# Kernel tuning notes

Hardware: AMD Instinct MI355X
Metric: run time of the kernel (lower is better)

Reference implementation:

```python
import jax, jax.numpy as jnp
import numpy as np

EMB_DIM = 768
NUM_HEADS = 12
OUT_DIM = 768


def setup_inputs() -> dict:
    key = jax.random.key(0)
    k_x, k_q, k_k, k_v, k_o = jax.random.split(key, 5)
    B, N, D = 8, 1024, EMB_DIM
    s = 1.0 / np.sqrt(D)
    return {
        "x": jax.random.normal(k_x, (B, N, D), dtype=jnp.float32),
        # torch nn.Linear weights are stored [out_features, in_features]
        "Wq": jax.random.normal(k_q, (D, D), dtype=jnp.float32) * s,
        "Wk": jax.random.normal(k_k, (D, D), dtype=jnp.float32) * s,
        "Wv": jax.random.normal(k_v, (D, D), dtype=jnp.float32) * s,
        "Wo": jax.random.normal(k_o, (OUT_DIM, D), dtype=jnp.float32) * s,
    }


def _split_heads(t, H):
    # [B, N, D] -> [B*H, N, D//H]  (heads folded into batch, per einsum 'b i d')
    B, N, D = t.shape
    return t.reshape(B, N, H, D // H).transpose(0, 2, 1, 3).reshape(B * H, N, D // H)


def _merge_heads(t, B, H):
    BH, N, dh = t.shape
    return t.reshape(B, H, N, dh).transpose(0, 2, 1, 3).reshape(B, N, H * dh)


def reference(x, Wq, Wk, Wv, Wo):
    B, N, D = x.shape
    H = NUM_HEADS
    dh = D // H
    # q/k/v projections (torch Linear: y = x @ W.T, no bias)
    q = _split_heads(x @ Wq.T, H)
    k = _split_heads(x @ Wk.T, H)
    v = _split_heads(x @ Wv.T, H)
    scale = dh ** (-0.5)
    # dots: 'b i d , b j d -> b i j' -> full [B*H, N, N] score matrix
    dots = jnp.einsum('bid,bjd->bij', q, k) * scale
    attn = jax.nn.softmax(dots, axis=-1)
    # dropout p=0.0 -> identity
    # vect: 'b i d , b d j -> b i j' == attn @ v
    vect = jnp.einsum('bij,bjd->bid', attn, v)
    out = _merge_heads(vect, B, H) @ Wo.T
    return out
```

## Files before the change

### kernel.cpp

```cpp
#include <hip/hip_runtime.h>
#include <hip/hip_bf16.h>
#include <stdint.h>


typedef __bf16 bf16x8 __attribute__((ext_vector_type(8)));
typedef __bf16 bf16x4 __attribute__((ext_vector_type(4)));
typedef float f32x4 __attribute__((ext_vector_type(4)));

#define GAS __attribute__((address_space(1)))
#define LAS __attribute__((address_space(3)))

__device__ __forceinline__ void glds16(const short* gp, short* lp) {
  __builtin_amdgcn_global_load_lds((const GAS void*)gp, (LAS void*)lp, 16, 0, 0);
}

__device__ __forceinline__ float fast_exp2(float x) {
#if __has_builtin(__builtin_amdgcn_exp2f)
  return __builtin_amdgcn_exp2f(x);
#else
  return __expf(x * 0.6931471805599453f);
#endif
}

__device__ __forceinline__ short bfbits(float f) {
  __bf16 b = (__bf16)f;
  union { __bf16 b; short s; } cv; cv.b = b;
  return cv.s;
}

__device__ __forceinline__ void stage8_f32(const float* __restrict__ src, short* dst) {
  float4 f0 = ((const float4*)src)[0];
  float4 f1 = ((const float4*)src)[1];
  bf16x8 t;
  t[0] = (__bf16)f0.x; t[1] = (__bf16)f0.y; t[2] = (__bf16)f0.z; t[3] = (__bf16)f0.w;
  t[4] = (__bf16)f1.x; t[5] = (__bf16)f1.y; t[6] = (__bf16)f1.z; t[7] = (__bf16)f1.w;
  *(bf16x8*)dst = t;
}

__global__ __launch_bounds__(256) void convert_kernel(
    const float* __restrict__ x, const float* __restrict__ Wq,
    const float* __restrict__ Wk, const float* __restrict__ Wv,
    const float* __restrict__ Wo,
    short* __restrict__ xb, short* __restrict__ wqkv, short* __restrict__ wob) {
  int u0 = blockIdx.x * 1024 + threadIdx.x;
#pragma unroll
  for (int i = 0; i < 4; ++i) {
    int u = u0 + i * 256;
    const float* src; short* dst;
    if (u < 786432) { src = x + (size_t)u * 8; dst = xb + (size_t)u * 8; }
    else if (u < 1007616) {
      int r = u - 786432;
      int wsel = r / 73728, off = r % 73728;
      const float* W = (wsel == 0) ? Wq : (wsel == 1) ? Wk : Wv;
      src = W + (size_t)off * 8;
      dst = wqkv + (size_t)r * 8;
    } else {
      int r = u - 1007616;
      src = Wo + (size_t)r * 8; dst = wob + (size_t)r * 8;
    }
    stage8_f32(src, dst);
  }
}

__device__ __forceinline__ void stage_half(const short* __restrict__ g, short* l,
                                           int w, int lane) {
#pragma unroll
  for (int p = 0; p < 2; ++p) {
    int c = (w * 2 + p) * 64 + lane;
    int row = c >> 3;
    int cs = ((c & 7) ^ (row & 7)) * 8;
    glds16(g + (size_t)row * 768 + cs, l + c * 8);
  }
}

__device__ __forceinline__ void stage_b192(const short* __restrict__ g, short* l,
                                           int w, int lane) {
#pragma unroll
  for (int p = 0; p < 3; ++p) {
    int c = (w * 3 + p) * 64 + lane;
    int row = c >> 3;
    int cs = ((c & 7) ^ (row & 7)) * 8;
    glds16(g + (size_t)row * 768 + cs, l + c * 8);
  }
}

__device__ __forceinline__ void bar_fence() {
  asm volatile("" ::: "memory");
  __builtin_amdgcn_s_barrier();
  asm volatile("" ::: "memory");
}

__device__ __forceinline__ void load_a8(const short* base, int wr, int l16, int quad,
                                        bf16x8 (&fa)[4][2]) {
#pragma unroll
  for (int mf = 0; mf < 4; ++mf)
#pragma unroll
    for (int kk = 0; kk < 2; ++kk) {
      int row = wr * 64 + mf * 16 + l16;
      fa[mf][kk] = *(const bf16x8*)&base[row * 64 + ((((kk << 2) + quad) ^ (row & 7)) << 3)];
    }
}

__device__ __forceinline__ void load_b4(const short* base, int rbase, int l16, int quad,
                                        bf16x8 (&fb)[2][2]) {
#pragma unroll
  for (int nf = 0; nf < 2; ++nf)
#pragma unroll
    for (int kk = 0; kk < 2; ++kk) {
      int row = rbase + nf * 16 + l16;
      fb[nf][kk] = *(const bf16x8*)&base[row * 64 + ((((kk << 2) + quad) ^ (row & 7)) << 3)];
    }
}

__device__ __forceinline__ void load_b2(const short* base, int rbase, int l16, int quad,
                                        bf16x8 (&fb)[2]) {
#pragma unroll
  for (int kk = 0; kk < 2; ++kk) {
    int row = rbase + l16;
    fb[kk] = *(const bf16x8*)&base[row * 64 + ((((kk << 2) + quad) ^ (row & 7)) << 3)];
  }
}

__device__ __forceinline__ void mma16(const bf16x8 (&fa)[4][2], const bf16x8 (&fb)[2][2],
                                      f32x4 (&acc)[4][4], int nf0) {
  __builtin_amdgcn_s_setprio(1);
#pragma unroll
  for (int kk = 0; kk < 2; ++kk)
#pragma unroll
    for (int mf = 0; mf < 4; ++mf)
#pragma unroll
      for (int nf = 0; nf < 2; ++nf)
        acc[mf][nf0 + nf] = __builtin_amdgcn_mfma_f32_16x16x32_bf16(
            fa[mf][kk], fb[nf][kk], acc[mf][nf0 + nf], 0, 0, 0);
  __builtin_amdgcn_s_setprio(0);
}

__device__ __forceinline__ void mma16o(const bf16x8 (&fa)[4][2], const bf16x8 (&fb)[2][2],
                                       f32x4 (&acc)[4][3]) {
  __builtin_amdgcn_s_setprio(1);
#pragma unroll
  for (int kk = 0; kk < 2; ++kk)
#pragma unroll
    for (int mf = 0; mf < 4; ++mf)
#pragma unroll
      for (int nf = 0; nf < 2; ++nf)
        acc[mf][nf] = __builtin_amdgcn_mfma_f32_16x16x32_bf16(
            fa[mf][kk], fb[nf][kk], acc[mf][nf], 0, 0, 0);
  __builtin_amdgcn_s_setprio(0);
}

__device__ __forceinline__ void mma8o(const bf16x8 (&fa)[4][2], const bf16x8 (&fb)[2],
                                      f32x4 (&acc)[4][3]) {
  __builtin_amdgcn_s_setprio(1);
#pragma unroll
  for (int kk = 0; kk < 2; ++kk)
#pragma unroll
    for (int mf = 0; mf < 4; ++mf)
      acc[mf][2] = __builtin_amdgcn_mfma_f32_16x16x32_bf16(
          fa[mf][kk], fb[kk], acc[mf][2], 0, 0, 0);
  __builtin_amdgcn_s_setprio(0);
}

__global__ __launch_bounds__(512, 4) void gemm_qkv(
    const short* __restrict__ xb, const short* __restrict__ wqkv,
    short* __restrict__ q, short* __restrict__ k, short* __restrict__ vt) {
  const int lin = blockIdx.x;
  const int xcd = lin & 7, grp = lin >> 3;
  const int by = grp >> 3;
  const int bx = xcd * 8 + (grp & 7);
  const int m0 = bx * 128;
  const int n0g = by * 256;
  const int tid = threadIdx.x;
  const int w = tid >> 6, lane = tid & 63, l16 = lane & 15, quad = lane >> 4;
  const int wr = w >> 2, wc = w & 3;

  __shared__ short sA[8192];
  __shared__ short sB[16384];

  const short* Asrc = xb + (size_t)m0 * 768;
  const short* Bsrc = wqkv + (size_t)n0g * 768;

  f32x4 acc[4][4];
#pragma unroll
  for (int i = 0; i < 4; ++i)
#pragma unroll
    for (int j = 0; j < 4; ++j) acc[i][j] = (f32x4){0.f, 0.f, 0.f, 0.f};

  const int bh = wc >> 1;
  const int rb0 = (wc & 1) * 64;

  for (int t = 0; t < 12; ++t) {
    __syncthreads();
    stage_half(Asrc + (size_t)t * 64, sA, w, lane);
    stage_half(Bsrc + (size_t)t * 64, sB, w, lane);
    stage_half(Bsrc + 98304 + (size_t)t * 64, &sB[8192], w, lane);
    __syncthreads();
    bf16x8 fa[4][2], fb0[2][2], fb1[2][2];
    load_a8(sA, wr, l16, quad, fa);
    load_b4(&sB[bh * 8192], rb0, l16, quad, fb0);
    mma16(fa, fb0, acc, 0);
    load_b4(&sB[bh * 8192], rb0 + 32, l16, quad, fb1);
    mma16(fa, fb1, acc, 2);
  }

  const int wsel = by / 3;
  const int nl0 = (by % 3) * 256 + wc * 64;
  if (wsel == 2) {
#pragma unroll
    for (int mf = 0; mf < 4; ++mf)
#pragma unroll
      for (int nf = 0; nf < 4; ++nf) {
        int token = m0 + wr * 64 + mf * 16 + quad * 4;
        int nl = nl0 + nf * 16 + l16;
        int bhh = (token >> 10) * 12 + (nl >> 6);
        int jt = (token >> 7) & 7;
        int fb = (wr * 2 + (mf >> 1)) * 4 + nf;
        short tmp[4];
#pragma unroll
        for (int r = 0; r < 4; ++r) tmp[r] = bfbits(acc[mf][nf][r]);
        *(uint2*)(vt + (size_t)bhh * 65536 + jt * 8192 + fb * 512 +
                  (l16 + 16 * quad) * 8 + (mf & 1) * 4) = *(const uint2*)tmp;
      }
  } else {
    short* C = wsel ? k : q;
    const float sc = wsel ? 1.0f : 0.1803368801111244f;
#pragma unroll
    for (int mf = 0; mf < 4; ++mf)
#pragma unroll
      for (int nf = 0; nf < 4; ++nf)
#pragma unroll
        for (int r = 0; r < 4; ++r) {
          int row = m0 + wr * 64 + mf * 16 + quad * 4 + r;
          int nl = nl0 + nf * 16 + l16;
          C[(size_t)row * 768 + nl] = bfbits(acc[mf][nf][r] * sc);
        }
  }
}

__device__ __forceinline__ void attn_stage_k(const short* __restrict__ kb, int j0,
                                             short* sK, int w, int lane) {
#pragma unroll
  for (int p = 0; p < 4; ++p) {
    int lin = (w * 4 + p) * 64 + lane;
    int row = lin >> 3;
    int cs = ((lin & 7) ^ (row & 7)) * 8;
    glds16(kb + (size_t)(j0 + row) * 768 + cs, &sK[lin * 8]);
  }
}

__device__ __forceinline__ void attn_stage_v(const short* __restrict__ vb, int jt,
                                             short* sVt, int w, int lane) {
#pragma unroll
  for (int p = 0; p < 4; ++p) {
    int c = (w * 4 + p) * 64 + lane;
    glds16(vb + (size_t)jt * 8192 + (size_t)c * 8, &sVt[c * 8]);
  }
}

__global__ __launch_bounds__(256, 3) void attn_kernel(
    const short* __restrict__ q, const short* __restrict__ k,
    const short* __restrict__ vt, short* __restrict__ vect) {
  const int bh = blockIdx.x % 96;
  const int qt = blockIdx.x / 96;
  const int b = bh / 12, h = bh % 12;
  const int m0 = qt * 128;
  const int tid = threadIdx.x;
  const int w = tid >> 6, lane = tid & 63, l16 = lane & 15, quad = lane >> 4;

  __shared__ short sK[128 * 64];
  __shared__ short sVt[64 * 128];

  const size_t base = (size_t)b * 786432 + (size_t)h * 64;
  const short* kb = k + base;
  const short* vb = vt + (size_t)bh * 65536;

#pragma unroll
  for (int p = 0; p < 4; ++p) {
    int lin = (w * 4 + p) * 64 + lane;
    int row = lin >> 3;
    int cs = ((lin & 7) ^ (row & 7)) * 8;
    glds16(q + base + (size_t)(m0 + row) * 768 + cs, &sK[lin * 8]);
  }
  asm volatile("s_waitcnt vmcnt(0)" ::: "memory");
  bar_fence();
  bf16x8 bq[2][2];
#pragma unroll
  for (int g = 0; g < 2; ++g)
#pragma unroll
    for (int kk = 0; kk < 2; ++kk) {
      int row = g * 64 + w * 16 + l16;
      bq[g][kk] = *(const bf16x8*)&sK[row * 64 + (((kk * 4 + quad) ^ (row & 7)) << 3)];
    }
  asm volatile("s_waitcnt lgkmcnt(0)" ::: "memory");
  __builtin_amdgcn_sched_barrier(0);
  bar_fence();

  attn_stage_k(kb, 0, sK, w, lane);
  attn_stage_v(vb, 0, sVt, w, lane);

  f32x4 l4[2];
  l4[0] = (f32x4){0.f, 0.f, 0.f, 0.f};
  l4[1] = (f32x4){0.f, 0.f, 0.f, 0.f};
  f32x4 oacc[2][4];
#pragma unroll
  for (int g = 0; g < 2; ++g)
#pragma unroll
    for (int td = 0; td < 4; ++td) oacc[g][td] = (f32x4){0.f, 0.f, 0.f, 0.f};

  for (int jt = 0; jt < 8; ++jt) {
    asm volatile("s_waitcnt vmcnt(4)" ::: "memory");
    bar_fence();

    bf16x4 pb[2][2][4];
#pragma unroll
    for (int jh = 0; jh < 2; ++jh) {
      f32x4 s[2][4];
#pragma unroll
      for (int g = 0; g < 2; ++g)
#pragma unroll
        for (int ti = 0; ti < 4; ++ti) s[g][ti] = (f32x4){0.f, 0.f, 0.f, 0.f};
      __builtin_amdgcn_s_setprio(1);
#pragma unroll
      for (int kk = 0; kk < 2; ++kk)
#pragma unroll
        for (int ti = 0; ti < 4; ++ti) {
          int row = jh * 64 + ti * 16 + l16;
          bf16x8 a = *(const bf16x8*)&sK[row * 64 + (((kk * 4 + quad) ^ (row & 7)) << 3)];
          s[0][ti] = __builtin_amdgcn_mfma_f32_16x16x32_bf16(a, bq[0][kk], s[0][ti], 0, 0, 0);
          s[1][ti] = __builtin_amdgcn_mfma_f32_16x16x32_bf16(a, bq[1][kk], s[1][ti], 0, 0, 0);
        }
      __builtin_amdgcn_s_setprio(0);
#pragma unroll
      for (int g = 0; g < 2; ++g)
#pragma unroll
        for (int ti = 0; ti < 4; ++ti) {
          f32x4 e;
          e[0] = fast_exp2(s[g][ti][0]);
          e[1] = fast_exp2(s[g][ti][1]);
          e[2] = fast_exp2(s[g][ti][2]);
          e[3] = fast_exp2(s[g][ti][3]);
          l4[g] += e;
          bf16x4 tb;
          tb[0] = (__bf16)e[0]; tb[1] = (__bf16)e[1];
          tb[2] = (__bf16)e[2]; tb[3] = (__bf16)e[3];
          pb[jh][g][ti] = tb;
        }
    }
    asm volatile("s_waitcnt lgkmcnt(0)" ::: "memory");
    __builtin_amdgcn_sched_barrier(0);
    bar_fence();
    if (jt < 7) attn_stage_k(kb, (jt + 1) * 128, sK, w, lane);

    if (jt < 7) { asm volatile("s_waitcnt vmcnt(4)" ::: "memory"); }
    else        { asm volatile("s_waitcnt vmcnt(0)" ::: "memory"); }
    bar_fence();

    __builtin_amdgcn_s_setprio(1);
#pragma unroll
    for (int jh = 0; jh < 2; ++jh)
#pragma unroll
      for (int t2 = 0; t2 < 2; ++t2) {
        union { bf16x4 hh[2]; bf16x8 v; } bp0, bp1;
        bp0.hh[0] = pb[jh][0][2 * t2];
        bp0.hh[1] = pb[jh][0][2 * t2 + 1];
        bp1.hh[0] = pb[jh][1][2 * t2];
        bp1.hh[1] = pb[jh][1][2 * t2 + 1];
        const int fb = (jh * 2 + t2) * 4;
#pragma unroll
        for (int td = 0; td < 4; ++td) {
          bf16x8 av = *(const bf16x8*)&sVt[(fb + td) * 512 + lane * 8];
          oacc[0][td] = __builtin_amdgcn_mfma_f32_16x16x32_bf16(av, bp0.v, oacc[0][td], 0, 0, 0);
          oacc[1][td] = __builtin_amdgcn_mfma_f32_16x16x32_bf16(av, bp1.v, oacc[1][td], 0, 0, 0);
        }
      }
    __builtin_amdgcn_s_setprio(0);
    asm volatile("s_waitcnt lgkmcnt(0)" ::: "memory");
    __builtin_amdgcn_sched_barrier(0);
    bar_fence();
    if (jt < 7) attn_stage_v(vb, jt + 1, sVt, w, lane);
  }

#pragma unroll
  for (int g = 0; g < 2; ++g) {
    float l = (l4[g][0] + l4[g][1]) + (l4[g][2] + l4[g][3]);
    l += __shfl_xor(l, 16);
    l += __shfl_xor(l, 32);
    float inv = 1.0f / l;
    int i_tok = m0 + g * 64 + w * 16 + l16;
#pragma unroll
    for (int td = 0; td < 4; ++td) {
      short tmp[4];
#pragma unroll
      for (int r = 0; r < 4; ++r) tmp[r] = bfbits(oacc[g][td][r] * inv);
      *(uint2*)(vect + base + (size_t)i_tok * 768 + td * 16 + quad * 4) = *(const uint2*)tmp;
    }
  }
}

__global__ __launch_bounds__(512, 2) void gemm_out(
    const short* __restrict__ vect, const short* __restrict__ wob,
    float* __restrict__ out) {
  const int lin = blockIdx.x;
  const int xcd = lin & 7, grp = lin >> 3;
  const int by = grp >> 3;
  const int bx = xcd * 8 + (grp & 7);
  const int m0 = bx * 128;
  const int n0g = by * 192;
  const int tid = threadIdx.x;
  const int w = tid >> 6, lane = tid & 63, l16 = lane & 15, quad = lane >> 4;
  const int wr = w >> 2, wc = w & 3;

  __shared__ short lds[3][20480];

  const short* Asrc = vect + (size_t)m0 * 768;
  const short* Bsrc = wob + (size_t)n0g * 768;

  f32x4 acc[4][3];
#pragma unroll
  for (int i = 0; i < 4; ++i)
#pragma unroll
    for (int j = 0; j < 3; ++j) acc[i][j] = (f32x4){0.f, 0.f, 0.f, 0.f};

  stage_half(Asrc, &lds[0][0], w, lane);
  stage_b192(Bsrc, &lds[0][8192], w, lane);
  stage_half(Asrc + 64, &lds[1][0], w, lane);
  stage_b192(Bsrc + 64, &lds[1][8192], w, lane);
  asm volatile("s_waitcnt vmcnt(5)" ::: "memory");
  bar_fence();

  const int rb0 = wc * 48;
  bf16x8 fa[4][2], fb01[2][2], fb2[2];

#pragma unroll
  for (int t = 0; t < 12; ++t) {
    const int buf = t % 3, nb = (t + 2) % 3;
    const bool pf = (t < 10);
    const short* A = &lds[buf][0];
    const short* Bb = &lds[buf][8192];

    load_a8(A, wr, l16, quad, fa);
    load_b4(Bb, rb0, l16, quad, fb01);
    if (pf) stage_half(Asrc + (size_t)(t + 2) * 64, &lds[nb][0], w, lane);
    bar_fence();
    __builtin_amdgcn_sched_barrier(0);
    mma16o(fa, fb01, acc);
    __builtin_amdgcn_sched_barrier(0);
    bar_fence();

    load_b2(Bb, rb0 + 32, l16, quad, fb2);
    if (pf) {
      stage_b192(Bsrc + (size_t)(t + 2) * 64, &lds[nb][8192], w, lane);
      asm volatile("s_waitcnt vmcnt(5)" ::: "memory");
    } else if (t == 10) {
      asm volatile("s_waitcnt vmcnt(0)" ::: "memory");
    }
    bar_fence();
    __builtin_amdgcn_sched_barrier(0);
    mma8o(fa, fb2, acc);
    __builtin_amdgcn_sched_barrier(0);
    bar_fence();
  }

#pragma unroll
  for (int mf = 0; mf < 4; ++mf)
#pragma unroll
    for (int nf = 0; nf < 3; ++nf)
#pragma unroll
      for (int r = 0; r < 4; ++r) {
        int row = m0 + wr * 64 + mf * 16 + quad * 4 + r;
        int col = n0g + wc * 48 + nf * 16 + l16;
        out[(size_t)row * 768 + col] = acc[mf][nf][r];
      }
}

extern "C" void kernel_launch(void* const* d_in, const int* in_sizes, int n_in,
                              void* d_out, int out_size, void* d_ws, size_t ws_size,
                              hipStream_t stream) {
  const float* x  = (const float*)d_in[0];
  const float* Wq = (const float*)d_in[1];
  const float* Wk = (const float*)d_in[2];
  const float* Wv = (const float*)d_in[3];
  const float* Wo = (const float*)d_in[4];
  float* out = (float*)d_out;

  const size_t MN = (size_t)8192 * 768;
  short* q    = (short*)d_ws;
  short* k    = q + MN;
  short* vt   = k + MN;
  short* vect = q;
  short* wob  = vt + MN;

  short* xb   = (short*)d_out;
  short* wqkv = xb + MN;

  convert_kernel<<<1056, 256, 0, stream>>>(x, Wq, Wk, Wv, Wo, xb, wqkv, wob);
  gemm_qkv<<<576, 512, 0, stream>>>(xb, wqkv, q, k, vt);
  attn_kernel<<<768, 256, 0, stream>>>(q, k, vt, vect);
  gemm_out<<<256, 512, 0, stream>>>(vect, wob, out);
}
```

Baseline: 170.5 us.

## Load V fragments directly from global into registers, dropping V LDS staging

The V tile is no longer staged through shared memory. Each wave now reads its pre-swizzled V fragments straight from global memory into registers before the PV MFMAs. This halves LDS use, which allows higher occupancy, and removes two barriers per iteration. In exchange, V global loads are no longer prefetched a tile ahead, so their latency is exposed, and every wave re-reads the same V data through cache.

```diff
diff --git a/kernel.cpp b/kernel.cpp
--- a/kernel.cpp
+++ b/kernel.cpp
@@ -248,15 +248,6 @@
   }
 }
 
-__device__ __forceinline__ void attn_stage_v(const short* __restrict__ vb, int jt,
-                                             short* sVt, int w, int lane) {
-#pragma unroll
-  for (int p = 0; p < 4; ++p) {
-    int c = (w * 4 + p) * 64 + lane;
-    glds16(vb + (size_t)jt * 8192 + (size_t)c * 8, &sVt[c * 8]);
-  }
-}
-
 __global__ __launch_bounds__(256, 3) void attn_kernel(
     const short* __restrict__ q, const short* __restrict__ k,
     const short* __restrict__ vt, short* __restrict__ vect) {
@@ -268,7 +259,6 @@
   const int w = tid >> 6, lane = tid & 63, l16 = lane & 15, quad = lane >> 4;
 
   __shared__ short sK[128 * 64];
-  __shared__ short sVt[64 * 128];
 
   const size_t base = (size_t)b * 786432 + (size_t)h * 64;
   const short* kb = k + base;
@@ -296,7 +286,6 @@
   bar_fence();
 
   attn_stage_k(kb, 0, sK, w, lane);
-  attn_stage_v(vb, 0, sVt, w, lane);
 
   f32x4 l4[2];
   l4[0] = (f32x4){0.f, 0.f, 0.f, 0.f};
@@ -308,7 +297,7 @@
     for (int td = 0; td < 4; ++td) oacc[g][td] = (f32x4){0.f, 0.f, 0.f, 0.f};
 
   for (int jt = 0; jt < 8; ++jt) {
-    asm volatile("s_waitcnt vmcnt(4)" ::: "memory");
+    asm volatile("s_waitcnt vmcnt(0)" ::: "memory");
     bar_fence();
 
     bf16x4 pb[2][2][4];
@@ -349,15 +338,18 @@
     asm volatile("s_waitcnt lgkmcnt(0)" ::: "memory");
     __builtin_amdgcn_sched_barrier(0);
     bar_fence();
-    if (jt < 7) attn_stage_k(kb, (jt + 1) * 128, sK, w, lane);
-
-    if (jt < 7) { asm volatile("s_waitcnt vmcnt(4)" ::: "memory"); }
-    else        { asm volatile("s_waitcnt vmcnt(0)" ::: "memory"); }
-    bar_fence();
-
-    __builtin_amdgcn_s_setprio(1);
-#pragma unroll
-    for (int jh = 0; jh < 2; ++jh)
+
+    const short* vj = vb + (size_t)jt * 8192;
+#pragma unroll
+    for (int jh = 0; jh < 2; ++jh) {
+      bf16x8 av[2][4];
+#pragma unroll
+      for (int t2 = 0; t2 < 2; ++t2)
+#pragma unroll
+        for (int td = 0; td < 4; ++td)
+          av[t2][td] = *(const bf16x8*)(vj + ((jh * 2 + t2) * 4 + td) * 512 + lane * 8);
+      if (jh == 0 && jt < 7) attn_stage_k(kb, (jt + 1) * 128, sK, w, lane);
+      __builtin_amdgcn_s_setprio(1);
 #pragma unroll
       for (int t2 = 0; t2 < 2; ++t2) {
         union { bf16x4 hh[2]; bf16x8 v; } bp0, bp1;
@@ -365,19 +357,14 @@
         bp0.hh[1] = pb[jh][0][2 * t2 + 1];
         bp1.hh[0] = pb[jh][1][2 * t2];
         bp1.hh[1] = pb[jh][1][2 * t2 + 1];
-        const int fb = (jh * 2 + t2) * 4;
 #pragma unroll
         for (int td = 0; td < 4; ++td) {
-          bf16x8 av = *(const bf16x8*)&sVt[(fb + td) * 512 + lane * 8];
-          oacc[0][td] = __builtin_amdgcn_mfma_f32_16x16x32_bf16(av, bp0.v, oacc[0][td], 0, 0, 0);
-          oacc[1][td] = __builtin_amdgcn_mfma_f32_16x16x32_bf16(av, bp1.v, oacc[1][td], 0, 0, 0);
+          oacc[0][td] = __builtin_amdgcn_mfma_f32_16x16x32_bf16(av[t2][td], bp0.v, oacc[0][td], 0, 0, 0);
+          oacc[1][td] = __builtin_amdgcn_mfma_f32_16x16x32_bf16(av[t2][td], bp1.v, oacc[1][td], 0, 0, 0);
         }
       }
-    __builtin_amdgcn_s_setprio(0);
-    asm volatile("s_waitcnt lgkmcnt(0)" ::: "memory");
-    __builtin_amdgcn_sched_barrier(0);
-    bar_fence();
-    if (jt < 7) attn_stage_v(vb, jt + 1, sVt, w, lane);
+      __builtin_amdgcn_s_setprio(0);
+    }
   }
 
 #pragma unroll
```

New measurement: 188.1 us. +10.3%, slower.
